# Performance work log

Measured on AMD Instinct MI355X. Metric: run time of the kernel, lower is better.

## Reference

```python
import jax, jax.numpy as jnp
import numpy as np

B, L, E, H, D = 4, 2048, 2048, 16, 128
HALF = D // 2
EPS = 1e-6


def setup_inputs() -> dict:
    key = jax.random.key(0)
    ks = jax.random.split(key, 8)
    s = 1.0 / np.sqrt(E)
    x = jax.random.normal(ks[0], (B, L, E), dtype=jnp.float32)
    # causal boolean mask, True = attend
    attention_mask = jnp.tril(jnp.ones((L, L), dtype=bool))[None, None, :, :]
    attention_mask = jnp.broadcast_to(attention_mask, (B, 1, L, L))
    pos = jnp.arange(L, dtype=jnp.float32)[:, None]
    inv_freq = 1.0 / (10000.0 ** (jnp.arange(HALF, dtype=jnp.float32) / HALF))
    ang = pos * inv_freq[None, :]  # [L, HALF]
    cos = jnp.broadcast_to(jnp.cos(ang)[None], (B, L, HALF)).astype(jnp.float32)
    sin = jnp.broadcast_to(jnp.sin(ang)[None], (B, L, HALF)).astype(jnp.float32)
    Wq = jax.random.normal(ks[1], (H * D, E), dtype=jnp.float32) * s
    Wk = jax.random.normal(ks[2], (H * D, E), dtype=jnp.float32) * s
    Wv = jax.random.normal(ks[3], (H * D, E), dtype=jnp.float32) * s
    Wo = jax.random.normal(ks[4], (E, H * D), dtype=jnp.float32) * s
    q_norm_w = jnp.ones((D,), dtype=jnp.float32)
    k_norm_w = jnp.ones((D,), dtype=jnp.float32)
    return {"x": x, "attention_mask": attention_mask, "cos": cos, "sin": sin,
            "Wq": Wq, "Wk": Wk, "Wv": Wv, "Wo": Wo,
            "q_norm_w": q_norm_w, "k_norm_w": k_norm_w}


def _rmsnorm(t, w):
    # t: [B,H,L,D]; matches torch: x / sqrt(mean(x^2) + eps) * w
    ms = jnp.mean(t * t, axis=-1, keepdims=True)
    return w * (t * jax.lax.rsqrt(ms + EPS))


def _rope(t, cos, sin):
    # t: [B,H,L,D]; cos/sin: [B,L,HALF] -> [B,1,L,HALF]
    c = cos[:, None, :, :]
    s = sin[:, None, :, :]
    t1, t2 = t[..., :HALF], t[..., HALF:]
    return jnp.concatenate([t1 * c - t2 * s, t1 * s + t2 * c], axis=-1)


def reference(x, attention_mask, cos, sin, Wq, Wk, Wv, Wo, q_norm_w, k_norm_w):
    b, l, _ = x.shape
    q = (x @ Wq.T).reshape(b, l, H, D).transpose(0, 2, 1, 3)  # [B,H,L,D]
    k = (x @ Wk.T).reshape(b, l, H, D).transpose(0, 2, 1, 3)
    v = (x @ Wv.T).reshape(b, l, H, D).transpose(0, 2, 1, 3)
    q = _rope(_rmsnorm(q, q_norm_w), cos, sin)
    k = _rope(_rmsnorm(k, k_norm_w), cos, sin)
    scale = 1.0 / jnp.sqrt(jnp.asarray(D, dtype=x.dtype))
    scores = jnp.einsum('bhld,bhmd->bhlm', q, k) * scale  # [B,H,L,L]
    scores = jnp.where(attention_mask, scores, -jnp.inf)
    attn = jax.nn.softmax(scores, axis=-1)
    out = jnp.einsum('bhlm,bhmd->bhld', attn, v)  # [B,H,L,D]
    out = out.transpose(0, 2, 1, 3).reshape(b, l, H * D)
    return out @ Wo.T
```

## Files before the change

### kernel.cpp

```cpp
#include <hip/hip_runtime.h>
#include <hip/hip_bf16.h>
#include <stdint.h>

#define B_SZ 4
#define L_SEQ 2048
#define EMB 2048
#define NH 16
#define HD 128
#define BLROWS (B_SZ * L_SEQ)
#define BK 32

typedef __bf16 bf16;
typedef __bf16 bf16x8 __attribute__((ext_vector_type(8)));
typedef __bf16 bf16x4 __attribute__((ext_vector_type(4)));
typedef float f32x4 __attribute__((ext_vector_type(4)));

#define MFMA16(A, Bv, C) __builtin_amdgcn_mfma_f32_16x16x32_bf16(A, Bv, C, 0, 0, 0)

__device__ __forceinline__ void gll16(bf16* l, const bf16* g) {
  __builtin_amdgcn_global_load_lds(
      (const __attribute__((address_space(1))) unsigned int*)g,
      (__attribute__((address_space(3))) unsigned int*)l, 16, 0, 0);
}

__global__ __launch_bounds__(256) void f2b_kernel(const float* __restrict__ in,
                                                  bf16* __restrict__ out, int n4) {
  int i = blockIdx.x * blockDim.x + threadIdx.x;
  int stride = gridDim.x * blockDim.x;
  for (; i < n4; i += stride) {
    float4 v = ((const float4*)in)[i];
    bf16x4 o = {(bf16)v.x, (bf16)v.y, (bf16)v.z, (bf16)v.w};
    ((bf16x4*)out)[i] = o;
  }
}

template <int EPI>
__global__ __launch_bounds__(512, 2) void gemm256(const bf16* __restrict__ A,
                                                  const bf16* __restrict__ Bm,
                                                  bf16* __restrict__ Cq,
                                                  bf16* __restrict__ Ck,
                                                  bf16* __restrict__ Cvt,
                                                  float* __restrict__ Cf,
                                                  int K) {
  __shared__ bf16 Abuf[3][256 * BK];
  __shared__ bf16 Bbuf[3][256 * BK];
  const int tid = threadIdx.x, lane = tid & 63, w = tid >> 6;
  const int wr = w >> 2, wc = w & 3;
  const int l15 = lane & 15;

  const int q8 = gridDim.x >> 3;
  const int wg = ((int)blockIdx.x & 7) * q8 + ((int)blockIdx.x >> 3);
  const int bm = (wg & 31) * 256;
  const int bn = (wg >> 5) * 256;
  const int NT = K / BK;

  const int idA0 = tid, idA1 = 512 + tid;
  const int ar0 = idA0 >> 2, ar1 = idA1 >> 2;
  const size_t aS0 = (size_t)(bm + ar0) * K + (((idA0 & 3) ^ ((ar0 >> 1) & 3)) * 8);
  const size_t aS1 = (size_t)(bm + ar1) * K + (((idA1 & 3) ^ ((ar1 >> 1) & 3)) * 8);
  const size_t bS0 = (size_t)(bn + ar0) * K + (((idA0 & 3) ^ ((ar0 >> 1) & 3)) * 8);
  const size_t bS1 = (size_t)(bn + ar1) * K + (((idA1 & 3) ^ ((ar1 >> 1) & 3)) * 8);
  const int ldsD0 = idA0 * 8, ldsD1 = idA1 * 8;

  const int eSw = ((lane >> 4) * 8) ^ (((l15 >> 1) & 3) << 3);
  int aoff[8], boff[4];
#pragma unroll
  for (int m = 0; m < 8; m++) aoff[m] = (wr * 128 + m * 16 + l15) * BK + eSw;
#pragma unroll
  for (int n = 0; n < 4; n++) boff[n] = (wc * 64 + n * 16 + l15) * BK + eSw;

  f32x4 acc[8][4] = {};

  gll16(&Abuf[0][ldsD0], A + aS0);
  gll16(&Bbuf[0][ldsD0], Bm + bS0);
  gll16(&Abuf[0][ldsD1], A + aS1);
  gll16(&Bbuf[0][ldsD1], Bm + bS1);
  gll16(&Abuf[1][ldsD0], A + aS0 + BK);
  gll16(&Bbuf[1][ldsD0], Bm + bS0 + BK);
  gll16(&Abuf[1][ldsD1], A + aS1 + BK);
  gll16(&Bbuf[1][ldsD1], Bm + bS1 + BK);
  asm volatile("s_waitcnt vmcnt(4)" ::: "memory");
  __builtin_amdgcn_s_barrier();
  asm volatile("" ::: "memory");

  int cur = 0, nxt = 2;
  for (int kt = 0; kt < NT; ++kt) {
    const bf16* __restrict__ Ab = Abuf[cur];
    const bf16* __restrict__ Bb = Bbuf[cur];
    const bool pre = (kt + 2 < NT);
    const size_t k2 = (size_t)(kt + 2) * BK;

    bf16x8 af[8], b0, b1;
#pragma unroll
    for (int m = 0; m < 8; m++) af[m] = *(const bf16x8*)&Ab[aoff[m]];
    b0 = *(const bf16x8*)&Bb[boff[0]];
    b1 = *(const bf16x8*)&Bb[boff[1]];
    if (pre) {
      gll16(&Abuf[nxt][ldsD0], A + aS0 + k2);
      gll16(&Bbuf[nxt][ldsD0], Bm + bS0 + k2);
    }
    asm volatile("s_waitcnt lgkmcnt(0)" ::: "memory");
    __builtin_amdgcn_sched_barrier(0);
    __builtin_amdgcn_s_setprio(1);
#pragma unroll
    for (int m = 0; m < 8; m++) acc[m][0] = MFMA16(af[m], b0, acc[m][0]);
#pragma unroll
    for (int m = 0; m < 8; m++) acc[m][1] = MFMA16(af[m], b1, acc[m][1]);
    __builtin_amdgcn_s_setprio(0);

    bf16x8 b2 = *(const bf16x8*)&Bb[boff[2]];
    bf16x8 b3 = *(const bf16x8*)&Bb[boff[3]];
    if (pre) {
      gll16(&Abuf[nxt][ldsD1], A + aS1 + k2);
      gll16(&Bbuf[nxt][ldsD1], Bm + bS1 + k2);
    }
    asm volatile("s_waitcnt lgkmcnt(0)" ::: "memory");
    __builtin_amdgcn_sched_barrier(0);
    __builtin_amdgcn_s_setprio(1);
#pragma unroll
    for (int m = 0; m < 8; m++) acc[m][2] = MFMA16(af[m], b2, acc[m][2]);
#pragma unroll
    for (int m = 0; m < 8; m++) acc[m][3] = MFMA16(af[m], b3, acc[m][3]);
    __builtin_amdgcn_s_setprio(0);

    if (kt < NT - 1) {
      if (pre)
        asm volatile("s_waitcnt vmcnt(4)" ::: "memory");
      else
        asm volatile("s_waitcnt vmcnt(0)" ::: "memory");
      __builtin_amdgcn_s_barrier();
      asm volatile("" ::: "memory");
    }
    cur = (cur == 2) ? 0 : cur + 1;
    nxt = (nxt == 2) ? 0 : nxt + 1;
  }

  const int grow0 = bm + wr * 128 + (lane >> 4) * 4;
  const int gcol0 = bn + wc * 64 + l15;
#pragma unroll
  for (int i = 0; i < 8; i++)
#pragma unroll
    for (int j = 0; j < 4; j++) {
      int grow = grow0 + i * 16;
      int gcol = gcol0 + j * 16;
      if (EPI == 1) {
#pragma unroll
        for (int r = 0; r < 4; r++)
          Cf[(size_t)(grow + r) * 2048 + gcol] = acc[i][j][r];
      } else {
        int mat = gcol >> 11, mcol = gcol & 2047;
        if (mat == 2) {
          int b = grow >> 11;
          bf16x4 pk = {(bf16)acc[i][j][0], (bf16)acc[i][j][1],
                       (bf16)acc[i][j][2], (bf16)acc[i][j][3]};
          *(bf16x4*)&Cvt[((size_t)(b * 2048 + mcol)) * 2048 + (grow & 2047)] = pk;
        } else {
          bf16* Cp = (mat == 0) ? Cq : Ck;
#pragma unroll
          for (int r = 0; r < 4; r++)
            Cp[(size_t)(grow + r) * 2048 + mcol] = (bf16)acc[i][j][r];
        }
      }
    }
}

__global__ __launch_bounds__(256) void normrope_kernel(bf16* __restrict__ T,
                                                       const float* __restrict__ w,
                                                       const float* __restrict__ cs,
                                                       const float* __restrict__ sn) {
  int row = blockIdx.x * 4 + (threadIdx.x >> 6);
  int lane = threadIdx.x & 63;
  int bl = row >> 4;
  int h = row & 15;
  bf16* p = T + (size_t)bl * EMB + h * HD;
  float v1 = (float)p[lane];
  float v2 = (float)p[lane + 64];
  float ss = v1 * v1 + v2 * v2;
#pragma unroll
  for (int m = 32; m; m >>= 1) ss += __shfl_xor(ss, m, 64);
  float r = rsqrtf(ss * (1.0f / 128.0f) + 1e-6f);
  float n1 = v1 * r * w[lane];
  float n2 = v2 * r * w[lane + 64];
  float c = cs[(size_t)bl * 64 + lane];
  float s = sn[(size_t)bl * 64 + lane];
  p[lane]      = (bf16)(n1 * c - n2 * s);
  p[lane + 64] = (bf16)(n1 * s + n2 * c);
}

__device__ __forceinline__ void stage_kv(bf16* Ksb, bf16* Vsb,
                                         const bf16* gK, const bf16* gV,
                                         int kt, int w, int lane) {
#pragma unroll
  for (int i = 0; i < 4; i++) {
    int ck = i * 256 + w * 64 + lane;
    int kr = ck >> 4, kc = ck & 15;
    gll16(&Ksb[ck * 8], gK + (size_t)(kt * 64 + kr) * EMB + ((kc ^ (kr & 7)) * 8));
    int dr = ck >> 3, vc = ck & 7;
    gll16(&Vsb[ck * 8], gV + (size_t)dr * L_SEQ + kt * 64 + ((vc ^ (dr & 7)) * 8));
  }
}

__global__ __launch_bounds__(256) void fattn_kernel(const bf16* __restrict__ Q,
                                                    const bf16* __restrict__ K,
                                                    const bf16* __restrict__ Vt,
                                                    bf16* __restrict__ AO) {
  __shared__ bf16 Ks[2][64 * 128];
  __shared__ bf16 Vs[2][64 * 128];
  __shared__ bf16 Ps[4 * 16 * 64];
  const int tid = threadIdx.x, lane = tid & 63, w = tid >> 6;

  int id = blockIdx.x + blockIdx.y * 32;
  int bh = id & 63;
  int qt = 31 - (id >> 6);
  const int b = bh >> 4, h = bh & 15;
  const size_t base = (size_t)b * L_SEQ * EMB + h * HD;
  const bf16* gK = K + base;
  const bf16* gV = Vt + (size_t)(b * NH + h) * HD * L_SEQ;
  const int qrow0 = qt * 64 + w * 16;

  const float a_ = 0.08838834764831845f * 1.4426950408889634f;
  const float b_ = 12.0f * 1.4426950408889634f;

  bf16x8 qf[4];
  {
    const bf16* qp = Q + base + (size_t)(qrow0 + (lane & 15)) * EMB + ((lane >> 4) * 8);
#pragma unroll
    for (int c = 0; c < 4; c++) qf[c] = *(const bf16x8*)(qp + c * 32);
  }
  const bf16 one1 = (bf16)1.0f;
  const bf16x8 ones = {one1, one1, one1, one1, one1, one1, one1, one1};

  f32x4 O[8] = {};
  f32x4 lsum = {0.f, 0.f, 0.f, 0.f};
  const int qg0 = qrow0 + (lane >> 4) * 4;
  bf16* myP = Ps + w * 1024;

  stage_kv(Ks[0], Vs[0], gK, gV, 0, w, lane);
  asm volatile("s_waitcnt vmcnt(0)" ::: "memory");
  __builtin_amdgcn_s_barrier();
  asm volatile("" ::: "memory");

  for (int kt = 0; kt <= qt; kt++) {
    const int cur = kt & 1;
    if (kt < qt) stage_kv(Ks[cur ^ 1], Vs[cur ^ 1], gK, gV, kt + 1, w, lane);

    f32x4 S[4] = {};
    __builtin_amdgcn_s_setprio(1);
#pragma unroll
    for (int s = 0; s < 4; s++) {
      int row = s * 16 + (lane & 15);
#pragma unroll
      for (int c = 0; c < 4; c++) {
        int swc = (c * 4 + (lane >> 4)) ^ (row & 7);
        bf16x8 kf = *(const bf16x8*)&Ks[cur][row * 128 + swc * 8];
        S[s] = MFMA16(qf[c], kf, S[s]);
      }
    }
    __builtin_amdgcn_s_setprio(0);

    const bool diag = (kt == qt);
    const int prow = (lane >> 4) * 4;
#pragma unroll
    for (int s = 0; s < 4; s++) {
      int kg = kt * 64 + s * 16 + (lane & 15);
#pragma unroll
      for (int r = 0; r < 4; r++) {
        float e = exp2f(S[s][r] * a_ - b_);
        if (diag && kg > qg0 + r) e = 0.f;
        int row = prow + r;
        myP[(row * 64 + s * 16 + (lane & 15)) ^ ((row & 7) << 3)] = (bf16)e;
      }
    }
    bf16x8 pf[2];
#pragma unroll
    for (int kk = 0; kk < 2; kk++) {
      int row = lane & 15;
      int swc = (kk * 4 + (lane >> 4)) ^ (row & 7);
      pf[kk] = *(const bf16x8*)&myP[row * 64 + swc * 8];
    }
    __builtin_amdgcn_s_setprio(1);
    lsum = MFMA16(pf[0], ones, lsum);
    lsum = MFMA16(pf[1], ones, lsum);
#pragma unroll
    for (int ni = 0; ni < 8; ni++) {
#pragma unroll
      for (int kk = 0; kk < 2; kk++) {
        int drow = ni * 16 + (lane & 15);
        int swc = (kk * 4 + (lane >> 4)) ^ (drow & 7);
        bf16x8 vf = *(const bf16x8*)&Vs[cur][drow * 64 + swc * 8];
        O[ni] = MFMA16(pf[kk], vf, O[ni]);
      }
    }
    __builtin_amdgcn_s_setprio(0);

    asm volatile("s_waitcnt vmcnt(0)" ::: "memory");
    __builtin_amdgcn_s_barrier();
    asm volatile("" ::: "memory");
  }

#pragma unroll
  for (int ni = 0; ni < 8; ni++) {
#pragma unroll
    for (int r = 0; r < 4; r++) {
      float o = O[ni][r] / lsum[r];
      AO[(size_t)(b * L_SEQ + qg0 + r) * EMB + h * HD + ni * 16 + (lane & 15)] = (bf16)o;
    }
  }
}

extern "C" void kernel_launch(void* const* d_in, const int* in_sizes, int n_in,
                              void* d_out, int out_size, void* d_ws, size_t ws_size,
                              hipStream_t stream) {
  const float* x = (const float*)d_in[0];
  const float* cosp = (const float*)d_in[2];
  const float* sinp = (const float*)d_in[3];
  const float* Wq = (const float*)d_in[4];
  const float* Wk = (const float*)d_in[5];
  const float* Wv = (const float*)d_in[6];
  const float* Wo = (const float*)d_in[7];
  const float* qw = (const float*)d_in[8];
  const float* kw = (const float*)d_in[9];

  const size_t ACT = (size_t)BLROWS * EMB * sizeof(bf16);
  const size_t WGT = (size_t)EMB * EMB * sizeof(bf16);
  char* ws = (char*)d_ws;
  bf16* xb    = (bf16*)ws;          ws += ACT;
  bf16* WQKVb = (bf16*)ws;          ws += 3 * WGT;
  bf16* Wob   = (bf16*)ws;          ws += WGT;
  bf16* Qb    = (bf16*)ws;          ws += ACT;
  bf16* Kb    = (bf16*)ws;          ws += ACT;
  bf16* Vtb   = (bf16*)ws;          ws += ACT;
  bf16* AOb   = (bf16*)ws;          ws += ACT;

  f2b_kernel<<<2048, 256, 0, stream>>>(x, xb, BLROWS * EMB / 4);
  f2b_kernel<<<1024, 256, 0, stream>>>(Wq, WQKVb, EMB * EMB / 4);
  f2b_kernel<<<1024, 256, 0, stream>>>(Wk, WQKVb + (size_t)EMB * EMB, EMB * EMB / 4);
  f2b_kernel<<<1024, 256, 0, stream>>>(Wv, WQKVb + 2 * (size_t)EMB * EMB, EMB * EMB / 4);
  f2b_kernel<<<1024, 256, 0, stream>>>(Wo, Wob, EMB * EMB / 4);

  gemm256<0><<<768, 512, 0, stream>>>(xb, WQKVb, Qb, Kb, Vtb, nullptr, EMB);

  normrope_kernel<<<BLROWS * NH / 4, 256, 0, stream>>>(Qb, qw, cosp, sinp);
  normrope_kernel<<<BLROWS * NH / 4, 256, 0, stream>>>(Kb, kw, cosp, sinp);

  fattn_kernel<<<dim3(32, B_SZ * NH), 256, 0, stream>>>(Qb, Kb, Vtb, AOb);

  gemm256<1><<<256, 512, 0, stream>>>(AOb, Wob, nullptr, nullptr, nullptr,
                                      (float*)d_out, EMB);
}
```

Measured before the change: 476.3 us.

## Switch GEMM mainloop to BK=64 double-buffered LDS with 8-way XOR swizzle

```diff
diff --git a/kernel.cpp b/kernel.cpp
--- a/kernel.cpp
+++ b/kernel.cpp
@@ -8,7 +8,6 @@
 #define NH 16
 #define HD 128
 #define BLROWS (B_SZ * L_SEQ)
-#define BK 32
 
 typedef __bf16 bf16;
 typedef __bf16 bf16x8 __attribute__((ext_vector_type(8)));
@@ -42,8 +41,8 @@
                                                   bf16* __restrict__ Cvt,
                                                   float* __restrict__ Cf,
                                                   int K) {
-  __shared__ bf16 Abuf[3][256 * BK];
-  __shared__ bf16 Bbuf[3][256 * BK];
+  __shared__ bf16 Abuf[2][256 * 64];
+  __shared__ bf16 Bbuf[2][256 * 64];
   const int tid = threadIdx.x, lane = tid & 63, w = tid >> 6;
   const int wr = w >> 2, wc = w & 3;
   const int l15 = lane & 15;
@@ -52,87 +51,95 @@
   const int wg = ((int)blockIdx.x & 7) * q8 + ((int)blockIdx.x >> 3);
   const int bm = (wg & 31) * 256;
   const int bn = (wg >> 5) * 256;
-  const int NT = K / BK;
-
-  const int idA0 = tid, idA1 = 512 + tid;
-  const int ar0 = idA0 >> 2, ar1 = idA1 >> 2;
-  const size_t aS0 = (size_t)(bm + ar0) * K + (((idA0 & 3) ^ ((ar0 >> 1) & 3)) * 8);
-  const size_t aS1 = (size_t)(bm + ar1) * K + (((idA1 & 3) ^ ((ar1 >> 1) & 3)) * 8);
-  const size_t bS0 = (size_t)(bn + ar0) * K + (((idA0 & 3) ^ ((ar0 >> 1) & 3)) * 8);
-  const size_t bS1 = (size_t)(bn + ar1) * K + (((idA1 & 3) ^ ((ar1 >> 1) & 3)) * 8);
-  const int ldsD0 = idA0 * 8, ldsD1 = idA1 * 8;
-
-  const int eSw = ((lane >> 4) * 8) ^ (((l15 >> 1) & 3) << 3);
-  int aoff[8], boff[4];
-#pragma unroll
-  for (int m = 0; m < 8; m++) aoff[m] = (wr * 128 + m * 16 + l15) * BK + eSw;
-#pragma unroll
-  for (int n = 0; n < 4; n++) boff[n] = (wc * 64 + n * 16 + l15) * BK + eSw;
+  const int NT = K >> 6;
+
+  size_t sAg[4], sBg[4];
+  int sdst[4];
+#pragma unroll
+  for (int g = 0; g < 4; g++) {
+    int id = g * 512 + tid;
+    int row = id >> 3, c = id & 7;
+    int scol = ((c ^ (row & 7)) * 8);
+    sAg[g] = (size_t)(bm + row) * K + scol;
+    sBg[g] = (size_t)(bn + row) * K + scol;
+    sdst[g] = id * 8;
+  }
+
+  int aoff[8][2], boff[4][2];
+#pragma unroll
+  for (int m = 0; m < 8; m++)
+#pragma unroll
+    for (int ks = 0; ks < 2; ks++) {
+      int row = wr * 128 + m * 16 + l15;
+      int cl = ks * 4 + (lane >> 4);
+      aoff[m][ks] = row * 64 + ((cl ^ (row & 7)) * 8);
+    }
+#pragma unroll
+  for (int n = 0; n < 4; n++)
+#pragma unroll
+    for (int ks = 0; ks < 2; ks++) {
+      int row = wc * 64 + n * 16 + l15;
+      int cl = ks * 4 + (lane >> 4);
+      boff[n][ks] = row * 64 + ((cl ^ (row & 7)) * 8);
+    }
 
   f32x4 acc[8][4] = {};
 
-  gll16(&Abuf[0][ldsD0], A + aS0);
-  gll16(&Bbuf[0][ldsD0], Bm + bS0);
-  gll16(&Abuf[0][ldsD1], A + aS1);
-  gll16(&Bbuf[0][ldsD1], Bm + bS1);
-  gll16(&Abuf[1][ldsD0], A + aS0 + BK);
-  gll16(&Bbuf[1][ldsD0], Bm + bS0 + BK);
-  gll16(&Abuf[1][ldsD1], A + aS1 + BK);
-  gll16(&Bbuf[1][ldsD1], Bm + bS1 + BK);
-  asm volatile("s_waitcnt vmcnt(4)" ::: "memory");
+#pragma unroll
+  for (int g = 0; g < 4; g++) {
+    gll16(&Abuf[0][sdst[g]], A + sAg[g]);
+    gll16(&Bbuf[0][sdst[g]], Bm + sBg[g]);
+  }
+  asm volatile("s_waitcnt vmcnt(0)" ::: "memory");
   __builtin_amdgcn_s_barrier();
   asm volatile("" ::: "memory");
 
-  int cur = 0, nxt = 2;
-  for (int kt = 0; kt < NT; ++kt) {
-    const bf16* __restrict__ Ab = Abuf[cur];
-    const bf16* __restrict__ Bb = Bbuf[cur];
-    const bool pre = (kt + 2 < NT);
-    const size_t k2 = (size_t)(kt + 2) * BK;
-
-    bf16x8 af[8], b0, b1;
-#pragma unroll
-    for (int m = 0; m < 8; m++) af[m] = *(const bf16x8*)&Ab[aoff[m]];
-    b0 = *(const bf16x8*)&Bb[boff[0]];
-    b1 = *(const bf16x8*)&Bb[boff[1]];
-    if (pre) {
-      gll16(&Abuf[nxt][ldsD0], A + aS0 + k2);
-      gll16(&Bbuf[nxt][ldsD0], Bm + bS0 + k2);
-    }
-    asm volatile("s_waitcnt lgkmcnt(0)" ::: "memory");
-    __builtin_amdgcn_sched_barrier(0);
-    __builtin_amdgcn_s_setprio(1);
-#pragma unroll
-    for (int m = 0; m < 8; m++) acc[m][0] = MFMA16(af[m], b0, acc[m][0]);
-#pragma unroll
-    for (int m = 0; m < 8; m++) acc[m][1] = MFMA16(af[m], b1, acc[m][1]);
-    __builtin_amdgcn_s_setprio(0);
-
-    bf16x8 b2 = *(const bf16x8*)&Bb[boff[2]];
-    bf16x8 b3 = *(const bf16x8*)&Bb[boff[3]];
-    if (pre) {
-      gll16(&Abuf[nxt][ldsD1], A + aS1 + k2);
-      gll16(&Bbuf[nxt][ldsD1], Bm + bS1 + k2);
-    }
-    asm volatile("s_waitcnt lgkmcnt(0)" ::: "memory");
-    __builtin_amdgcn_sched_barrier(0);
-    __builtin_amdgcn_s_setprio(1);
-#pragma unroll
-    for (int m = 0; m < 8; m++) acc[m][2] = MFMA16(af[m], b2, acc[m][2]);
-#pragma unroll
-    for (int m = 0; m < 8; m++) acc[m][3] = MFMA16(af[m], b3, acc[m][3]);
-    __builtin_amdgcn_s_setprio(0);
-
-    if (kt < NT - 1) {
-      if (pre)
-        asm volatile("s_waitcnt vmcnt(4)" ::: "memory");
-      else
-        asm volatile("s_waitcnt vmcnt(0)" ::: "memory");
+  for (int t = 0; t < NT; ++t) {
+    const bf16* __restrict__ Ab = Abuf[t & 1];
+    const bf16* __restrict__ Bb = Bbuf[t & 1];
+    bf16* __restrict__ An = Abuf[(t + 1) & 1];
+    bf16* __restrict__ Bn = Bbuf[(t + 1) & 1];
+    const size_t k1 = (size_t)(t + 1) << 6;
+    const bool pre = (t + 1 < NT);
+
+    bf16x8 bq[4][2];
+
+#pragma unroll
+    for (int mp = 0; mp < 4; mp++) {
+      bf16x8 a0k0 = *(const bf16x8*)&Ab[aoff[2 * mp][0]];
+      bf16x8 a0k1 = *(const bf16x8*)&Ab[aoff[2 * mp][1]];
+      bf16x8 a1k0 = *(const bf16x8*)&Ab[aoff[2 * mp + 1][0]];
+      bf16x8 a1k1 = *(const bf16x8*)&Ab[aoff[2 * mp + 1][1]];
+      if (mp == 0) {
+#pragma unroll
+        for (int n = 0; n < 4; n++) {
+          bq[n][0] = *(const bf16x8*)&Bb[boff[n][0]];
+          bq[n][1] = *(const bf16x8*)&Bb[boff[n][1]];
+        }
+        if (pre) {
+#pragma unroll
+          for (int g = 0; g < 4; g++) {
+            gll16(&An[sdst[g]], A + sAg[g] + k1);
+            gll16(&Bn[sdst[g]], Bm + sBg[g] + k1);
+          }
+        }
+      }
+      __builtin_amdgcn_s_barrier();
+      asm volatile("s_waitcnt lgkmcnt(0)" ::: "memory");
+      __builtin_amdgcn_sched_barrier(0);
+      __builtin_amdgcn_s_setprio(1);
+#pragma unroll
+      for (int n = 0; n < 4; n++) {
+        acc[2 * mp][n] = MFMA16(a0k0, bq[n][0], acc[2 * mp][n]);
+        acc[2 * mp][n] = MFMA16(a0k1, bq[n][1], acc[2 * mp][n]);
+        acc[2 * mp + 1][n] = MFMA16(a1k0, bq[n][0], acc[2 * mp + 1][n]);
+        acc[2 * mp + 1][n] = MFMA16(a1k1, bq[n][1], acc[2 * mp + 1][n]);
+      }
+      __builtin_amdgcn_s_setprio(0);
+      if (mp == 3) asm volatile("s_waitcnt vmcnt(0)" ::: "memory");
       __builtin_amdgcn_s_barrier();
       asm volatile("" ::: "memory");
     }
-    cur = (cur == 2) ? 0 : cur + 1;
-    nxt = (nxt == 2) ? 0 : nxt + 1;
   }
 
   const int grow0 = bm + wr * 128 + (lane >> 4) * 4;
```

Result: slower. 491.7 us (+3.2%).

## Enlarge attention query tile to 128 rows, two 16-row subtiles per wave

Applied to the files above, without the earlier changes.

```diff
diff --git a/kernel.cpp b/kernel.cpp
--- a/kernel.cpp
+++ b/kernel.cpp
@@ -206,92 +206,106 @@
                                                     bf16* __restrict__ AO) {
   __shared__ bf16 Ks[2][64 * 128];
   __shared__ bf16 Vs[2][64 * 128];
-  __shared__ bf16 Ps[4 * 16 * 64];
+  __shared__ bf16 Ps[4 * 32 * 64];
   const int tid = threadIdx.x, lane = tid & 63, w = tid >> 6;
-
-  int id = blockIdx.x + blockIdx.y * 32;
+  const int l15 = lane & 15;
+
+  int id = blockIdx.x + blockIdx.y * 16;
   int bh = id & 63;
-  int qt = 31 - (id >> 6);
+  int qti = 15 - (id >> 6);
   const int b = bh >> 4, h = bh & 15;
   const size_t base = (size_t)b * L_SEQ * EMB + h * HD;
   const bf16* gK = K + base;
   const bf16* gV = Vt + (size_t)(b * NH + h) * HD * L_SEQ;
-  const int qrow0 = qt * 64 + w * 16;
+  const int qrow0 = qti * 128 + w * 32;
 
   const float a_ = 0.08838834764831845f * 1.4426950408889634f;
   const float b_ = 12.0f * 1.4426950408889634f;
 
-  bf16x8 qf[4];
-  {
-    const bf16* qp = Q + base + (size_t)(qrow0 + (lane & 15)) * EMB + ((lane >> 4) * 8);
-#pragma unroll
-    for (int c = 0; c < 4; c++) qf[c] = *(const bf16x8*)(qp + c * 32);
+  bf16x8 qf[2][4];
+#pragma unroll
+  for (int mi = 0; mi < 2; mi++) {
+    const bf16* qp = Q + base + (size_t)(qrow0 + mi * 16 + l15) * EMB + ((lane >> 4) * 8);
+#pragma unroll
+    for (int c = 0; c < 4; c++) qf[mi][c] = *(const bf16x8*)(qp + c * 32);
   }
   const bf16 one1 = (bf16)1.0f;
   const bf16x8 ones = {one1, one1, one1, one1, one1, one1, one1, one1};
 
-  f32x4 O[8] = {};
-  f32x4 lsum = {0.f, 0.f, 0.f, 0.f};
-  const int qg0 = qrow0 + (lane >> 4) * 4;
-  bf16* myP = Ps + w * 1024;
-
+  f32x4 O[2][8] = {};
+  f32x4 lsum[2] = {};
+  const int prow = (lane >> 4) * 4;
+  bf16* myP = Ps + w * 2048;
+
+  const int nkt = 2 * qti + 2;
   stage_kv(Ks[0], Vs[0], gK, gV, 0, w, lane);
   asm volatile("s_waitcnt vmcnt(0)" ::: "memory");
   __builtin_amdgcn_s_barrier();
   asm volatile("" ::: "memory");
 
-  for (int kt = 0; kt <= qt; kt++) {
+  for (int kt = 0; kt < nkt; kt++) {
     const int cur = kt & 1;
-    if (kt < qt) stage_kv(Ks[cur ^ 1], Vs[cur ^ 1], gK, gV, kt + 1, w, lane);
-
-    f32x4 S[4] = {};
-    __builtin_amdgcn_s_setprio(1);
-#pragma unroll
-    for (int s = 0; s < 4; s++) {
-      int row = s * 16 + (lane & 15);
-#pragma unroll
-      for (int c = 0; c < 4; c++) {
-        int swc = (c * 4 + (lane >> 4)) ^ (row & 7);
-        bf16x8 kf = *(const bf16x8*)&Ks[cur][row * 128 + swc * 8];
-        S[s] = MFMA16(qf[c], kf, S[s]);
-      }
-    }
-    __builtin_amdgcn_s_setprio(0);
-
-    const bool diag = (kt == qt);
-    const int prow = (lane >> 4) * 4;
-#pragma unroll
-    for (int s = 0; s < 4; s++) {
-      int kg = kt * 64 + s * 16 + (lane & 15);
-#pragma unroll
-      for (int r = 0; r < 4; r++) {
-        float e = exp2f(S[s][r] * a_ - b_);
-        if (diag && kg > qg0 + r) e = 0.f;
-        int row = prow + r;
-        myP[(row * 64 + s * 16 + (lane & 15)) ^ ((row & 7) << 3)] = (bf16)e;
-      }
-    }
-    bf16x8 pf[2];
-#pragma unroll
-    for (int kk = 0; kk < 2; kk++) {
-      int row = lane & 15;
-      int swc = (kk * 4 + (lane >> 4)) ^ (row & 7);
-      pf[kk] = *(const bf16x8*)&myP[row * 64 + swc * 8];
-    }
-    __builtin_amdgcn_s_setprio(1);
-    lsum = MFMA16(pf[0], ones, lsum);
-    lsum = MFMA16(pf[1], ones, lsum);
-#pragma unroll
-    for (int ni = 0; ni < 8; ni++) {
-#pragma unroll
-      for (int kk = 0; kk < 2; kk++) {
-        int drow = ni * 16 + (lane & 15);
-        int swc = (kk * 4 + (lane >> 4)) ^ (drow & 7);
-        bf16x8 vf = *(const bf16x8*)&Vs[cur][drow * 64 + swc * 8];
-        O[ni] = MFMA16(pf[kk], vf, O[ni]);
-      }
-    }
-    __builtin_amdgcn_s_setprio(0);
+    if (kt + 1 < nkt) stage_kv(Ks[cur ^ 1], Vs[cur ^ 1], gK, gV, kt + 1, w, lane);
+
+    const bool active = (kt * 64 <= qrow0 + 31);
+    if (active) {
+      f32x4 S[2][4] = {};
+      __builtin_amdgcn_s_setprio(1);
+#pragma unroll
+      for (int s = 0; s < 4; s++) {
+        int row = s * 16 + l15;
+#pragma unroll
+        for (int c = 0; c < 4; c++) {
+          int swc = (c * 4 + (lane >> 4)) ^ (row & 7);
+          bf16x8 kf = *(const bf16x8*)&Ks[cur][row * 128 + swc * 8];
+          S[0][s] = MFMA16(qf[0][c], kf, S[0][s]);
+          S[1][s] = MFMA16(qf[1][c], kf, S[1][s]);
+        }
+      }
+      __builtin_amdgcn_s_setprio(0);
+
+#pragma unroll
+      for (int mi = 0; mi < 2; mi++)
+#pragma unroll
+        for (int s = 0; s < 4; s++) {
+          int kg = kt * 64 + s * 16 + l15;
+#pragma unroll
+          for (int r = 0; r < 4; r++) {
+            int qg = qrow0 + mi * 16 + prow + r;
+            float e = exp2f(S[mi][s][r] * a_ - b_);
+            if (kg > qg) e = 0.f;
+            int row = mi * 16 + prow + r;
+            myP[(row * 64 + s * 16 + l15) ^ ((row & 7) << 3)] = (bf16)e;
+          }
+        }
+      bf16x8 pf[2][2];
+#pragma unroll
+      for (int mi = 0; mi < 2; mi++)
+#pragma unroll
+        for (int kk = 0; kk < 2; kk++) {
+          int row = mi * 16 + l15;
+          int swc = (kk * 4 + (lane >> 4)) ^ (row & 7);
+          pf[mi][kk] = *(const bf16x8*)&myP[row * 64 + swc * 8];
+        }
+      __builtin_amdgcn_s_setprio(1);
+#pragma unroll
+      for (int mi = 0; mi < 2; mi++) {
+        lsum[mi] = MFMA16(pf[mi][0], ones, lsum[mi]);
+        lsum[mi] = MFMA16(pf[mi][1], ones, lsum[mi]);
+      }
+#pragma unroll
+      for (int ni = 0; ni < 8; ni++) {
+#pragma unroll
+        for (int kk = 0; kk < 2; kk++) {
+          int drow = ni * 16 + l15;
+          int swc = (kk * 4 + (lane >> 4)) ^ (drow & 7);
+          bf16x8 vf = *(const bf16x8*)&Vs[cur][drow * 64 + swc * 8];
+          O[0][ni] = MFMA16(pf[0][kk], vf, O[0][ni]);
+          O[1][ni] = MFMA16(pf[1][kk], vf, O[1][ni]);
+        }
+      }
+      __builtin_amdgcn_s_setprio(0);
+    }
 
     asm volatile("s_waitcnt vmcnt(0)" ::: "memory");
     __builtin_amdgcn_s_barrier();
@@ -299,13 +313,16 @@
   }
 
 #pragma unroll
-  for (int ni = 0; ni < 8; ni++) {
-#pragma unroll
-    for (int r = 0; r < 4; r++) {
-      float o = O[ni][r] / lsum[r];
-      AO[(size_t)(b * L_SEQ + qg0 + r) * EMB + h * HD + ni * 16 + (lane & 15)] = (bf16)o;
-    }
-  }
+  for (int mi = 0; mi < 2; mi++)
+#pragma unroll
+    for (int ni = 0; ni < 8; ni++) {
+#pragma unroll
+      for (int r = 0; r < 4; r++) {
+        float o = O[mi][ni][r] / lsum[mi][r];
+        int grow = qrow0 + mi * 16 + prow + r;
+        AO[(size_t)(b * L_SEQ + grow) * EMB + h * HD + ni * 16 + l15] = (bf16)o;
+      }
+    }
 }
 
 extern "C" void kernel_launch(void* const* d_in, const int* in_sizes, int n_in,
@@ -343,7 +360,7 @@
   normrope_kernel<<<BLROWS * NH / 4, 256, 0, stream>>>(Qb, qw, cosp, sinp);
   normrope_kernel<<<BLROWS * NH / 4, 256, 0, stream>>>(Kb, kw, cosp, sinp);
 
-  fattn_kernel<<<dim3(32, B_SZ * NH), 256, 0, stream>>>(Qb, Kb, Vtb, AOb);
+  fattn_kernel<<<dim3(16, B_SZ * NH), 256, 0, stream>>>(Qb, Kb, Vtb, AOb);
 
   gemm256<1><<<256, 512, 0, stream>>>(AOb, Wob, nullptr, nullptr, nullptr,
                                       (float*)d_out, EMB);
```

Measured after the change: 529.8 us. 11.2% more time.

## Merge weight-cast and norm-rope launches, use 256x128 tiles for output GEMM

Applied to the files above, without the earlier changes.

```diff
diff --git a/kernel.cpp b/kernel.cpp
--- a/kernel.cpp
+++ b/kernel.cpp
@@ -34,7 +34,28 @@
   }
 }
 
-template <int EPI>
+__global__ __launch_bounds__(256) void f2bW_kernel(const float* __restrict__ w0,
+                                                   const float* __restrict__ w1,
+                                                   const float* __restrict__ w2,
+                                                   const float* __restrict__ w3,
+                                                   bf16* __restrict__ o0,
+                                                   bf16* __restrict__ o1,
+                                                   bf16* __restrict__ o2,
+                                                   bf16* __restrict__ o3, int n4) {
+  const float* in = (blockIdx.y == 0) ? w0 : (blockIdx.y == 1) ? w1
+                    : (blockIdx.y == 2) ? w2 : w3;
+  bf16* out = (blockIdx.y == 0) ? o0 : (blockIdx.y == 1) ? o1
+              : (blockIdx.y == 2) ? o2 : o3;
+  int i = blockIdx.x * blockDim.x + threadIdx.x;
+  int stride = gridDim.x * blockDim.x;
+  for (; i < n4; i += stride) {
+    float4 v = ((const float4*)in)[i];
+    bf16x4 o = {(bf16)v.x, (bf16)v.y, (bf16)v.z, (bf16)v.w};
+    ((bf16x4*)out)[i] = o;
+  }
+}
+
+template <int EPI, int BNT>
 __global__ __launch_bounds__(512, 2) void gemm256(const bf16* __restrict__ A,
                                                   const bf16* __restrict__ Bm,
                                                   bf16* __restrict__ Cq,
@@ -42,16 +63,18 @@
                                                   bf16* __restrict__ Cvt,
                                                   float* __restrict__ Cf,
                                                   int K) {
+  constexpr int NB = BNT / 64;
   __shared__ bf16 Abuf[3][256 * BK];
-  __shared__ bf16 Bbuf[3][256 * BK];
+  __shared__ bf16 Bbuf[3][BNT * BK];
   const int tid = threadIdx.x, lane = tid & 63, w = tid >> 6;
   const int wr = w >> 2, wc = w & 3;
   const int l15 = lane & 15;
 
   const int q8 = gridDim.x >> 3;
   const int wg = ((int)blockIdx.x & 7) * q8 + ((int)blockIdx.x >> 3);
-  const int bm = (wg & 31) * 256;
-  const int bn = (wg >> 5) * 256;
+  const int nbm = 32;
+  const int bm = (wg & (nbm - 1)) * 256;
+  const int bn = (wg / nbm) * BNT;
   const int NT = K / BK;
 
   const int idA0 = tid, idA1 = 512 + tid;
@@ -63,23 +86,26 @@
   const int ldsD0 = idA0 * 8, ldsD1 = idA1 * 8;
 
   const int eSw = ((lane >> 4) * 8) ^ (((l15 >> 1) & 3) << 3);
-  int aoff[8], boff[4];
+  int aoff[8], boff[NB];
 #pragma unroll
   for (int m = 0; m < 8; m++) aoff[m] = (wr * 128 + m * 16 + l15) * BK + eSw;
 #pragma unroll
-  for (int n = 0; n < 4; n++) boff[n] = (wc * 64 + n * 16 + l15) * BK + eSw;
-
-  f32x4 acc[8][4] = {};
+  for (int n = 0; n < NB; n++) boff[n] = (wc * (BNT / 4) + n * 16 + l15) * BK + eSw;
+
+  f32x4 acc[8][NB] = {};
 
   gll16(&Abuf[0][ldsD0], A + aS0);
   gll16(&Bbuf[0][ldsD0], Bm + bS0);
   gll16(&Abuf[0][ldsD1], A + aS1);
-  gll16(&Bbuf[0][ldsD1], Bm + bS1);
+  if constexpr (BNT == 256) gll16(&Bbuf[0][ldsD1], Bm + bS1);
   gll16(&Abuf[1][ldsD0], A + aS0 + BK);
   gll16(&Bbuf[1][ldsD0], Bm + bS0 + BK);
   gll16(&Abuf[1][ldsD1], A + aS1 + BK);
-  gll16(&Bbuf[1][ldsD1], Bm + bS1 + BK);
-  asm volatile("s_waitcnt vmcnt(4)" ::: "memory");
+  if constexpr (BNT == 256) gll16(&Bbuf[1][ldsD1], Bm + bS1 + BK);
+  if constexpr (BNT == 256)
+    asm volatile("s_waitcnt vmcnt(4)" ::: "memory");
+  else
+    asm volatile("s_waitcnt vmcnt(3)" ::: "memory");
   __builtin_amdgcn_s_barrier();
   asm volatile("" ::: "memory");
 
@@ -90,11 +116,11 @@
     const bool pre = (kt + 2 < NT);
     const size_t k2 = (size_t)(kt + 2) * BK;
 
-    bf16x8 af[8], b0, b1;
+    bf16x8 af[8], bq[NB];
 #pragma unroll
     for (int m = 0; m < 8; m++) af[m] = *(const bf16x8*)&Ab[aoff[m]];
-    b0 = *(const bf16x8*)&Bb[boff[0]];
-    b1 = *(const bf16x8*)&Bb[boff[1]];
+    bq[0] = *(const bf16x8*)&Bb[boff[0]];
+    if constexpr (NB > 2) bq[1] = *(const bf16x8*)&Bb[boff[1]];
     if (pre) {
       gll16(&Abuf[nxt][ldsD0], A + aS0 + k2);
       gll16(&Bbuf[nxt][ldsD0], Bm + bS0 + k2);
@@ -103,31 +129,41 @@
     __builtin_amdgcn_sched_barrier(0);
     __builtin_amdgcn_s_setprio(1);
 #pragma unroll
-    for (int m = 0; m < 8; m++) acc[m][0] = MFMA16(af[m], b0, acc[m][0]);
-#pragma unroll
-    for (int m = 0; m < 8; m++) acc[m][1] = MFMA16(af[m], b1, acc[m][1]);
+    for (int m = 0; m < 8; m++) acc[m][0] = MFMA16(af[m], bq[0], acc[m][0]);
+    if constexpr (NB > 2) {
+#pragma unroll
+      for (int m = 0; m < 8; m++) acc[m][1] = MFMA16(af[m], bq[1], acc[m][1]);
+    }
     __builtin_amdgcn_s_setprio(0);
 
-    bf16x8 b2 = *(const bf16x8*)&Bb[boff[2]];
-    bf16x8 b3 = *(const bf16x8*)&Bb[boff[3]];
+    constexpr int n2 = (NB > 2) ? 2 : 1;
+    bf16x8 b2 = *(const bf16x8*)&Bb[boff[n2]];
+    bf16x8 b3;
+    if constexpr (NB > 2) b3 = *(const bf16x8*)&Bb[boff[3]];
     if (pre) {
       gll16(&Abuf[nxt][ldsD1], A + aS1 + k2);
-      gll16(&Bbuf[nxt][ldsD1], Bm + bS1 + k2);
+      if constexpr (BNT == 256) gll16(&Bbuf[nxt][ldsD1], Bm + bS1 + k2);
     }
     asm volatile("s_waitcnt lgkmcnt(0)" ::: "memory");
     __builtin_amdgcn_sched_barrier(0);
     __builtin_amdgcn_s_setprio(1);
 #pragma unroll
-    for (int m = 0; m < 8; m++) acc[m][2] = MFMA16(af[m], b2, acc[m][2]);
-#pragma unroll
-    for (int m = 0; m < 8; m++) acc[m][3] = MFMA16(af[m], b3, acc[m][3]);
+    for (int m = 0; m < 8; m++) acc[m][n2] = MFMA16(af[m], b2, acc[m][n2]);
+    if constexpr (NB > 2) {
+#pragma unroll
+      for (int m = 0; m < 8; m++) acc[m][3] = MFMA16(af[m], b3, acc[m][3]);
+    }
     __builtin_amdgcn_s_setprio(0);
 
     if (kt < NT - 1) {
-      if (pre)
-        asm volatile("s_waitcnt vmcnt(4)" ::: "memory");
-      else
+      if (pre) {
+        if constexpr (BNT == 256)
+          asm volatile("s_waitcnt vmcnt(4)" ::: "memory");
+        else
+          asm volatile("s_waitcnt vmcnt(3)" ::: "memory");
+      } else {
         asm volatile("s_waitcnt vmcnt(0)" ::: "memory");
+      }
       __builtin_amdgcn_s_barrier();
       asm volatile("" ::: "memory");
     }
@@ -136,11 +172,11 @@
   }
 
   const int grow0 = bm + wr * 128 + (lane >> 4) * 4;
-  const int gcol0 = bn + wc * 64 + l15;
+  const int gcol0 = bn + wc * (BNT / 4) + l15;
 #pragma unroll
   for (int i = 0; i < 8; i++)
 #pragma unroll
-    for (int j = 0; j < 4; j++) {
+    for (int j = 0; j < NB; j++) {
       int grow = grow0 + i * 16;
       int gcol = gcol0 + j * 16;
       if (EPI == 1) {
@@ -164,10 +200,14 @@
     }
 }
 
-__global__ __launch_bounds__(256) void normrope_kernel(bf16* __restrict__ T,
-                                                       const float* __restrict__ w,
-                                                       const float* __restrict__ cs,
-                                                       const float* __restrict__ sn) {
+__global__ __launch_bounds__(256) void normrope2_kernel(bf16* __restrict__ Tq,
+                                                        bf16* __restrict__ Tk,
+                                                        const float* __restrict__ wq,
+                                                        const float* __restrict__ wk,
+                                                        const float* __restrict__ cs,
+                                                        const float* __restrict__ sn) {
+  bf16* T = blockIdx.y ? Tk : Tq;
+  const float* w = blockIdx.y ? wk : wq;
   int row = blockIdx.x * 4 + (threadIdx.x >> 6);
   int lane = threadIdx.x & 63;
   int bl = row >> 4;
@@ -333,18 +373,17 @@
   bf16* AOb   = (bf16*)ws;          ws += ACT;
 
   f2b_kernel<<<2048, 256, 0, stream>>>(x, xb, BLROWS * EMB / 4);
-  f2b_kernel<<<1024, 256, 0, stream>>>(Wq, WQKVb, EMB * EMB / 4);
-  f2b_kernel<<<1024, 256, 0, stream>>>(Wk, WQKVb + (size_t)EMB * EMB, EMB * EMB / 4);
-  f2b_kernel<<<1024, 256, 0, stream>>>(Wv, WQKVb + 2 * (size_t)EMB * EMB, EMB * EMB / 4);
-  f2b_kernel<<<1024, 256, 0, stream>>>(Wo, Wob, EMB * EMB / 4);
-
-  gemm256<0><<<768, 512, 0, stream>>>(xb, WQKVb, Qb, Kb, Vtb, nullptr, EMB);
-
-  normrope_kernel<<<BLROWS * NH / 4, 256, 0, stream>>>(Qb, qw, cosp, sinp);
-  normrope_kernel<<<BLROWS * NH / 4, 256, 0, stream>>>(Kb, kw, cosp, sinp);
+  f2bW_kernel<<<dim3(512, 4), 256, 0, stream>>>(
+      Wq, Wk, Wv, Wo, WQKVb, WQKVb + (size_t)EMB * EMB,
+      WQKVb + 2 * (size_t)EMB * EMB, Wob, EMB * EMB / 4);
+
+  gemm256<0, 256><<<768, 512, 0, stream>>>(xb, WQKVb, Qb, Kb, Vtb, nullptr, EMB);
+
+  normrope2_kernel<<<dim3(BLROWS * NH / 4, 2), 256, 0, stream>>>(Qb, Kb, qw, kw,
+                                                                 cosp, sinp);
 
   fattn_kernel<<<dim3(32, B_SZ * NH), 256, 0, stream>>>(Qb, Kb, Vtb, AOb);
 
-  gemm256<1><<<256, 512, 0, stream>>>(AOb, Wob, nullptr, nullptr, nullptr,
-                                      (float*)d_out, EMB);
-}
+  gemm256<1, 128><<<512, 512, 0, stream>>>(AOb, Wob, nullptr, nullptr, nullptr,
+                                           (float*)d_out, EMB);
+}
```

Measured after the change: 478.8 us. About the same (+0.5%).
